# Kernel tuning notes

Hardware: AMD Instinct MI355X
Metric: run time of the kernel (lower is better)

## Reference

```python
import jax
import jax.numpy as jnp
from jax import lax
import numpy as np

B, T, IN, H, K = 8, 4096, 512, 512, 2


def setup_inputs() -> dict:
    key = jax.random.key(0)
    k = jax.random.split(key, 5)
    scale_w0 = 1.0 / np.sqrt(IN * K)
    scale_w1 = 1.0 / np.sqrt(H * K)
    return {
        "x": jax.random.normal(k[0], (B, T, IN), jnp.float32),
        "w0": jax.random.normal(k[1], (3 * H, IN, K), jnp.float32) * scale_w0,
        "b0": jax.random.normal(k[2], (3 * H,), jnp.float32) * scale_w0,
        "w1": jax.random.normal(k[3], (3 * H, H, K), jnp.float32) * scale_w1,
        "b1": jax.random.normal(k[4], (3 * H,), jnp.float32) * scale_w1,
    }


def _qrnn_layer(x, w, b):
    # x: [B, T, C]; w: [3H, C, K]; causal conv (left pad K-1), matching
    # torch padding=K-1 then slicing off the last K-1 timesteps.
    xc = jnp.transpose(x, (0, 2, 1))  # [B, C, T]
    conv = lax.conv_general_dilated(
        xc, w, window_strides=(1,), padding=[(K - 1, 0)],
        dimension_numbers=("NCH", "OIH", "NCH"))
    conv = conv + b[None, :, None]
    conv = jnp.transpose(conv, (0, 2, 1))  # [B, T, 3H]
    z, f, o = jnp.split(conv, 3, axis=-1)
    z = jnp.tanh(z)
    f = jax.nn.sigmoid(f)
    o = jax.nn.sigmoid(o)

    def step(h, zfo):
        zt, ft, ot = zfo
        h = ft * h + (1.0 - ft) * zt  # fo-pool recurrence
        return h, ot * h

    h0 = jnp.zeros((x.shape[0], z.shape[-1]), x.dtype)
    hT, outs = lax.scan(
        step, h0,
        (jnp.swapaxes(z, 0, 1), jnp.swapaxes(f, 0, 1), jnp.swapaxes(o, 0, 1)))
    return jnp.swapaxes(outs, 0, 1), hT  # [B, T, H], [B, H]


def reference(x, w0, b0, w1, b1):
    out, h0 = _qrnn_layer(x, w0, b0)
    out, h1 = _qrnn_layer(out, w1, b1)
    return out, h0, h1
```

## Files before the change

### kernel.cpp

```cpp
#include <hip/hip_runtime.h>
#include <cstdint>

#define B_ 8
#define T_ 4096
#define TP1 4097
#define IN_ 512
#define H_ 512
#define N3H 1536
#define KD 1024
#define CHUNKS 64
#define CLEN 64

typedef __attribute__((ext_vector_type(4))) float floatx4;
typedef __attribute__((ext_vector_type(4))) float f4;
typedef __attribute__((ext_vector_type(8))) short short8;
typedef __attribute__((ext_vector_type(4))) unsigned short us4;
typedef __attribute__((ext_vector_type(4))) _Float16 h4;

__device__ __forceinline__ unsigned short f2bf(float v){
  unsigned int u = __float_as_uint(v);
  unsigned int r = (u + 0x7fffu + ((u >> 16) & 1u)) >> 16;
  return (unsigned short)r;
}
__device__ __forceinline__ float sigm(float x){ return 1.f/(1.f + __expf(-x)); }
__device__ __forceinline__ float tanhf_(float x){ return 2.f*sigm(2.f*x) - 1.f; }

__global__ void cast_pad_kernel(const float* __restrict__ x, unsigned short* __restrict__ xpad){
  int64_t i = (int64_t)blockIdx.x*256 + threadIdx.x;
  const int64_t total = (int64_t)B_*TP1*(IN_/4);
  if (i >= total) return;
  int cg = (int)(i & 127);
  int64_t r = i >> 7;
  int t = (int)(r % TP1);
  int b = (int)(r / TP1);
  us4 o;
  if (t == 0){ o = (us4){0,0,0,0}; }
  else {
    f4 v = *(const f4*)(x + ((int64_t)b*T_ + (t-1))*IN_ + cg*4);
    #pragma unroll
    for (int u=0;u<4;++u) o[u] = f2bf(v[u]);
  }
  *(us4*)(xpad + r*IN_ + cg*4) = o;
}

__global__ void wt_kernel(const float* __restrict__ w, unsigned short* __restrict__ wt){
  int i = blockIdx.x*256 + threadIdx.x;
  if (i >= N3H*512) return;
  int ci = i & 511;
  int o = i >> 9;
  const float* wp = w + (int64_t)o*KD + ci*2;
  wt[(int64_t)o*KD + ci]       = f2bf(wp[0]);
  wt[(int64_t)o*KD + 512 + ci] = f2bf(wp[1]);
}

__global__ __launch_bounds__(256) void gemm_kernel(
    const unsigned short* __restrict__ A, const unsigned short* __restrict__ W,
    const float* __restrict__ bias, _Float16* __restrict__ C){
  __shared__ unsigned short As[128*32];
  __shared__ unsigned short Bs[128*32];
  const int tid = threadIdx.x;
  const int lane = tid & 63;
  const int wave = tid >> 6;
  const int bid = blockIdx.x;
  const int xcd = bid & 7;
  const int kb  = bid >> 3;
  const int colt = kb % 12;
  const int rowt = (kb / 12) * 8 + xcd;
  const int m0 = rowt * 128;
  const int n0 = colt * 128;
  const int bb = m0 / T_;
  const int act = n0 >> 9;
  const unsigned short* aSrc = A + (int64_t)(m0 + bb + (tid>>2))*IN_ + (tid&3)*8;
  const unsigned short* bSrc = W + (int64_t)(n0 + (tid>>2))*KD + (tid&3)*8;
  unsigned short* aDst = As + tid*8;
  unsigned short* bDst = Bs + tid*8;
  const int wm = wave & 1;
  const int wn = wave >> 1;
  const int l16 = lane & 15;
  const int quad = lane >> 4;
  floatx4 acc[4][4];
  #pragma unroll
  for (int i=0;i<4;i++)
    #pragma unroll
    for (int j=0;j<4;j++) acc[i][j] = (floatx4){0.f,0.f,0.f,0.f};
  const unsigned short* aLds = As + (wm*64 + l16)*32 + quad*8;
  const unsigned short* bLds = Bs + (wn*64 + l16)*32 + quad*8;

  for (int kk = 0; kk < KD; kk += 32){
    __syncthreads();
    __builtin_amdgcn_global_load_lds((const __attribute__((address_space(1))) void*)(aSrc + kk),
                                     (__attribute__((address_space(3))) void*)(aDst), 16, 0, 0);
    __builtin_amdgcn_global_load_lds((const __attribute__((address_space(1))) void*)(aSrc + 64*IN_ + kk),
                                     (__attribute__((address_space(3))) void*)(aDst + 2048), 16, 0, 0);
    __builtin_amdgcn_global_load_lds((const __attribute__((address_space(1))) void*)(bSrc + kk),
                                     (__attribute__((address_space(3))) void*)(bDst), 16, 0, 0);
    __builtin_amdgcn_global_load_lds((const __attribute__((address_space(1))) void*)(bSrc + 64*KD + kk),
                                     (__attribute__((address_space(3))) void*)(bDst + 2048), 16, 0, 0);
    __syncthreads();
    short8 af[4], bfr[4];
    #pragma unroll
    for (int i=0;i<4;i++) af[i] = *(const short8*)(aLds + i*16*32);
    #pragma unroll
    for (int j=0;j<4;j++) bfr[j] = *(const short8*)(bLds + j*16*32);
    #pragma unroll
    for (int i=0;i<4;i++)
      #pragma unroll
      for (int j=0;j<4;j++)
        acc[i][j] = __builtin_amdgcn_mfma_f32_16x16x32_bf16(af[i], bfr[j], acc[i][j], 0, 0, 0);
  }
  float bv[4];
  #pragma unroll
  for (int j=0;j<4;j++) bv[j] = bias[n0 + wn*64 + j*16 + l16];
  #pragma unroll
  for (int i=0;i<4;i++){
    int row = m0 + wm*64 + i*16 + quad*4;
    #pragma unroll
    for (int j=0;j<4;j++){
      int col = n0 + wn*64 + j*16 + l16;
      _Float16* cp = C + (int64_t)row*N3H + col;
      #pragma unroll
      for (int r=0;r<4;r++){
        float v = acc[i][j][r] + bv[j];
        v = (act == 0) ? tanhf_(v) : sigm(v);
        cp[(int64_t)r*N3H] = (_Float16)v;
      }
    }
  }
}

__global__ void scan_phase1(const _Float16* __restrict__ conv,
                            float* __restrict__ carA, float* __restrict__ carB){
  int q = blockIdx.x*256 + threadIdx.x;
  int chg = q & 127;
  int bq = (q >> 7) & 7;
  int c  = q >> 10;
  int ch = chg*4;
  f4 Aa = {1.f,1.f,1.f,1.f}, Bb = {0.f,0.f,0.f,0.f};
  const _Float16* p = conv + ((int64_t)bq*T_ + c*CLEN)*N3H + ch;
  for (int s=0;s<CLEN;++s){
    h4 zh = *(const h4*)p;
    h4 fh = *(const h4*)(p+512);
    #pragma unroll
    for (int u=0;u<4;++u){
      float fv = (float)fh[u];
      float zv = (float)zh[u];
      Aa[u] *= fv;
      Bb[u] = fv*Bb[u] + (1.f-fv)*zv;
    }
    p += N3H;
  }
  *(f4*)(carA + (int64_t)q*4) = Aa;
  *(f4*)(carB + (int64_t)q*4) = Bb;
}

__global__ void scan_phase2(const float* __restrict__ carA, const float* __restrict__ carB,
                            float* __restrict__ hstart, float* __restrict__ hT){
  int q = blockIdx.x*256 + threadIdx.x;
  f4 h = {0.f,0.f,0.f,0.f};
  for (int c=0;c<CHUNKS;++c){
    int64_t idx = (int64_t)c*4096 + q*4;
    *(f4*)(hstart + idx) = h;
    f4 a = *(const f4*)(carA + idx);
    f4 b = *(const f4*)(carB + idx);
    #pragma unroll
    for (int u=0;u<4;++u) h[u] = a[u]*h[u] + b[u];
  }
  *(f4*)(hT + (int64_t)q*4) = h;
}

template<int LAYER>
__global__ void scan_phase3(const _Float16* __restrict__ conv,
                            const float* __restrict__ hstart, unsigned short* __restrict__ xpad,
                            float* __restrict__ outf){
  int q = blockIdx.x*256 + threadIdx.x;
  int chg = q & 127;
  int bq = (q >> 7) & 7;
  int c  = q >> 10;
  int ch = chg*4;
  f4 h = *(const f4*)(hstart + (int64_t)q*4);
  const _Float16* p = conv + ((int64_t)bq*T_ + c*CLEN)*N3H + ch;
  int t = c*CLEN;
  for (int s=0;s<CLEN;++s){
    h4 zh = *(const h4*)p;
    h4 fh = *(const h4*)(p+512);
    h4 oh = *(const h4*)(p+1024);
    if (LAYER == 0){
      us4 ov4;
      #pragma unroll
      for (int u=0;u<4;++u){
        float fv = (float)fh[u];
        h[u] = fv*h[u] + (1.f-fv)*(float)zh[u];
        ov4[u] = f2bf((float)oh[u]*h[u]);
      }
      *(us4*)(xpad + ((int64_t)bq*TP1 + t + 1)*IN_ + ch) = ov4;
    } else {
      f4 of4;
      #pragma unroll
      for (int u=0;u<4;++u){
        float fv = (float)fh[u];
        h[u] = fv*h[u] + (1.f-fv)*(float)zh[u];
        of4[u] = (float)oh[u]*h[u];
      }
      *(f4*)(outf + ((int64_t)bq*T_ + t)*H_ + ch) = of4;
    }
    ++t; p += N3H;
  }
}

extern "C" void kernel_launch(void* const* d_in, const int* in_sizes, int n_in,
                              void* d_out, int out_size, void* d_ws, size_t ws_size,
                              hipStream_t stream){
  const float* x  = (const float*)d_in[0];
  const float* w0 = (const float*)d_in[1];
  const float* b0 = (const float*)d_in[2];
  const float* w1 = (const float*)d_in[3];
  const float* b1 = (const float*)d_in[4];
  float* out = (float*)d_out;

  char* ws = (char*)d_ws;
  size_t off = 0;
  auto alloc = [&](size_t bytes)->char*{
    char* p = ws + off; off = (off + bytes + 255) & ~(size_t)255; return p; };
  unsigned short* xpad = (unsigned short*)alloc((size_t)B_*TP1*IN_*2);
  unsigned short* Wt0  = (unsigned short*)alloc((size_t)N3H*KD*2);
  unsigned short* Wt1  = (unsigned short*)alloc((size_t)N3H*KD*2);
  _Float16* conv = (_Float16*)alloc((size_t)B_*T_*N3H*2);
  float* carA = (float*)alloc((size_t)CHUNKS*4096*4);
  float* carB = (float*)alloc((size_t)CHUNKS*4096*4);
  float* hst  = (float*)alloc((size_t)CHUNKS*4096*4);
  if (off > ws_size) return;

  float* out_main = out;
  float* h0 = out + (int64_t)B_*T_*H_;
  float* h1 = h0 + B_*H_;

  const int64_t padN = (int64_t)B_*TP1*(IN_/4);
  cast_pad_kernel<<<(int)((padN + 255)/256), 256, 0, stream>>>(x, xpad);
  wt_kernel<<<(N3H*512 + 255)/256, 256, 0, stream>>>(w0, Wt0);
  wt_kernel<<<(N3H*512 + 255)/256, 256, 0, stream>>>(w1, Wt1);

  const int ggrid = (N3H/128) * ((B_*T_)/128);
  gemm_kernel<<<ggrid, 256, 0, stream>>>(xpad, Wt0, b0, conv);
  scan_phase1<<<256, 256, 0, stream>>>(conv, carA, carB);
  scan_phase2<<<4, 256, 0, stream>>>(carA, carB, hst, h0);
  scan_phase3<0><<<256, 256, 0, stream>>>(conv, hst, xpad, nullptr);

  gemm_kernel<<<ggrid, 256, 0, stream>>>(xpad, Wt1, b1, conv);
  scan_phase1<<<256, 256, 0, stream>>>(conv, carA, carB);
  scan_phase2<<<4, 256, 0, stream>>>(carA, carB, hst, h1);
  scan_phase3<1><<<256, 256, 0, stream>>>(conv, hst, nullptr, out_main);
}
```

Measured before the change: 491.2 us.

## Double scan chunks, batch scan loads, widen GEMM K-step, merge weight casts

Splits the time scan into 128 chunks of 32 steps so the scan kernels launch twice as many blocks. The scan loops now issue 8 timesteps of loads before computing, to expose memory-level parallelism. The GEMM stages 64 K-elements per barrier pair using two LDS buffers, halving synchronisation count. The two weight-cast launches are fused into one via a 2D grid. Phase2 does twice as many serial steps and LDS use doubles.

Measured after the change: 499.3 us. No clear change (+1.6%).

```diff
diff --git a/kernel.cpp b/kernel.cpp
--- a/kernel.cpp
+++ b/kernel.cpp
@@ -8,8 +8,8 @@
 #define H_ 512
 #define N3H 1536
 #define KD 1024
-#define CHUNKS 64
-#define CLEN 64
+#define CHUNKS 128
+#define CLEN 32
 
 typedef __attribute__((ext_vector_type(4))) float floatx4;
 typedef __attribute__((ext_vector_type(4))) float f4;
@@ -24,6 +24,10 @@
 }
 __device__ __forceinline__ float sigm(float x){ return 1.f/(1.f + __expf(-x)); }
 __device__ __forceinline__ float tanhf_(float x){ return 2.f*sigm(2.f*x) - 1.f; }
+
+#define GLLS(src, dst) __builtin_amdgcn_global_load_lds( \
+    (const __attribute__((address_space(1))) void*)(src), \
+    (__attribute__((address_space(3))) void*)(dst), 16, 0, 0)
 
 __global__ void cast_pad_kernel(const float* __restrict__ x, unsigned short* __restrict__ xpad){
   int64_t i = (int64_t)blockIdx.x*256 + threadIdx.x;
@@ -43,9 +47,12 @@
   *(us4*)(xpad + r*IN_ + cg*4) = o;
 }
 
-__global__ void wt_kernel(const float* __restrict__ w, unsigned short* __restrict__ wt){
+__global__ void wt_kernel(const float* __restrict__ wA, unsigned short* __restrict__ wtA,
+                          const float* __restrict__ wB, unsigned short* __restrict__ wtB){
   int i = blockIdx.x*256 + threadIdx.x;
   if (i >= N3H*512) return;
+  const float* w = blockIdx.y ? wB : wA;
+  unsigned short* wt = blockIdx.y ? wtB : wtA;
   int ci = i & 511;
   int o = i >> 9;
   const float* wp = w + (int64_t)o*KD + ci*2;
@@ -56,8 +63,8 @@
 __global__ __launch_bounds__(256) void gemm_kernel(
     const unsigned short* __restrict__ A, const unsigned short* __restrict__ W,
     const float* __restrict__ bias, _Float16* __restrict__ C){
-  __shared__ unsigned short As[128*32];
-  __shared__ unsigned short Bs[128*32];
+  __shared__ unsigned short As[2][128*32];
+  __shared__ unsigned short Bs[2][128*32];
   const int tid = threadIdx.x;
   const int lane = tid & 63;
   const int wave = tid >> 6;
@@ -72,8 +79,10 @@
   const int act = n0 >> 9;
   const unsigned short* aSrc = A + (int64_t)(m0 + bb + (tid>>2))*IN_ + (tid&3)*8;
   const unsigned short* bSrc = W + (int64_t)(n0 + (tid>>2))*KD + (tid&3)*8;
-  unsigned short* aDst = As + tid*8;
-  unsigned short* bDst = Bs + tid*8;
+  unsigned short* aDst0 = As[0] + tid*8;
+  unsigned short* aDst1 = As[1] + tid*8;
+  unsigned short* bDst0 = Bs[0] + tid*8;
+  unsigned short* bDst1 = Bs[1] + tid*8;
   const int wm = wave & 1;
   const int wn = wave >> 1;
   const int l16 = lane & 15;
@@ -83,30 +92,35 @@
   for (int i=0;i<4;i++)
     #pragma unroll
     for (int j=0;j<4;j++) acc[i][j] = (floatx4){0.f,0.f,0.f,0.f};
-  const unsigned short* aLds = As + (wm*64 + l16)*32 + quad*8;
-  const unsigned short* bLds = Bs + (wn*64 + l16)*32 + quad*8;
-
-  for (int kk = 0; kk < KD; kk += 32){
+  const int fragOff = (wm*64 + l16)*32 + quad*8;
+  const int fragOffB = (wn*64 + l16)*32 + quad*8;
+
+  for (int kk = 0; kk < KD; kk += 64){
     __syncthreads();
-    __builtin_amdgcn_global_load_lds((const __attribute__((address_space(1))) void*)(aSrc + kk),
-                                     (__attribute__((address_space(3))) void*)(aDst), 16, 0, 0);
-    __builtin_amdgcn_global_load_lds((const __attribute__((address_space(1))) void*)(aSrc + 64*IN_ + kk),
-                                     (__attribute__((address_space(3))) void*)(aDst + 2048), 16, 0, 0);
-    __builtin_amdgcn_global_load_lds((const __attribute__((address_space(1))) void*)(bSrc + kk),
-                                     (__attribute__((address_space(3))) void*)(bDst), 16, 0, 0);
-    __builtin_amdgcn_global_load_lds((const __attribute__((address_space(1))) void*)(bSrc + 64*KD + kk),
-                                     (__attribute__((address_space(3))) void*)(bDst + 2048), 16, 0, 0);
+    GLLS(aSrc + kk,             aDst0);
+    GLLS(aSrc + 64*IN_ + kk,    aDst0 + 2048);
+    GLLS(aSrc + kk + 32,        aDst1);
+    GLLS(aSrc + 64*IN_ + kk+32, aDst1 + 2048);
+    GLLS(bSrc + kk,             bDst0);
+    GLLS(bSrc + 64*KD + kk,     bDst0 + 2048);
+    GLLS(bSrc + kk + 32,        bDst1);
+    GLLS(bSrc + 64*KD + kk+32,  bDst1 + 2048);
     __syncthreads();
-    short8 af[4], bfr[4];
-    #pragma unroll
-    for (int i=0;i<4;i++) af[i] = *(const short8*)(aLds + i*16*32);
-    #pragma unroll
-    for (int j=0;j<4;j++) bfr[j] = *(const short8*)(bLds + j*16*32);
-    #pragma unroll
-    for (int i=0;i<4;i++)
-      #pragma unroll
-      for (int j=0;j<4;j++)
-        acc[i][j] = __builtin_amdgcn_mfma_f32_16x16x32_bf16(af[i], bfr[j], acc[i][j], 0, 0, 0);
+    #pragma unroll
+    for (int s=0;s<2;++s){
+      const unsigned short* aLds = As[s] + fragOff;
+      const unsigned short* bLds = Bs[s] + fragOffB;
+      short8 af[4], bfr[4];
+      #pragma unroll
+      for (int i=0;i<4;i++) af[i] = *(const short8*)(aLds + i*16*32);
+      #pragma unroll
+      for (int j=0;j<4;j++) bfr[j] = *(const short8*)(bLds + j*16*32);
+      #pragma unroll
+      for (int i=0;i<4;i++)
+        #pragma unroll
+        for (int j=0;j<4;j++)
+          acc[i][j] = __builtin_amdgcn_mfma_f32_16x16x32_bf16(af[i], bfr[j], acc[i][j], 0, 0, 0);
+    }
   }
   float bv[4];
   #pragma unroll
@@ -137,17 +151,24 @@
   int ch = chg*4;
   f4 Aa = {1.f,1.f,1.f,1.f}, Bb = {0.f,0.f,0.f,0.f};
   const _Float16* p = conv + ((int64_t)bq*T_ + c*CLEN)*N3H + ch;
-  for (int s=0;s<CLEN;++s){
-    h4 zh = *(const h4*)p;
-    h4 fh = *(const h4*)(p+512);
-    #pragma unroll
-    for (int u=0;u<4;++u){
-      float fv = (float)fh[u];
-      float zv = (float)zh[u];
-      Aa[u] *= fv;
-      Bb[u] = fv*Bb[u] + (1.f-fv)*zv;
-    }
-    p += N3H;
+  for (int g=0; g<CLEN/8; ++g){
+    h4 zb[8], fb[8];
+    #pragma unroll
+    for (int u=0;u<8;++u){
+      zb[u] = *(const h4*)(p + (int64_t)u*N3H);
+      fb[u] = *(const h4*)(p + (int64_t)u*N3H + 512);
+    }
+    #pragma unroll
+    for (int u=0;u<8;++u){
+      #pragma unroll
+      for (int v=0;v<4;++v){
+        float fv = (float)fb[u][v];
+        float zv = (float)zb[u][v];
+        Aa[v] *= fv;
+        Bb[v] = fv*Bb[v] + (1.f-fv)*zv;
+      }
+    }
+    p += (int64_t)8*N3H;
   }
   *(f4*)(carA + (int64_t)q*4) = Aa;
   *(f4*)(carB + (int64_t)q*4) = Bb;
@@ -157,13 +178,21 @@
                             float* __restrict__ hstart, float* __restrict__ hT){
   int q = blockIdx.x*256 + threadIdx.x;
   f4 h = {0.f,0.f,0.f,0.f};
-  for (int c=0;c<CHUNKS;++c){
-    int64_t idx = (int64_t)c*4096 + q*4;
-    *(f4*)(hstart + idx) = h;
-    f4 a = *(const f4*)(carA + idx);
-    f4 b = *(const f4*)(carB + idx);
-    #pragma unroll
-    for (int u=0;u<4;++u) h[u] = a[u]*h[u] + b[u];
+  for (int g=0; g<CHUNKS/8; ++g){
+    f4 av[8], bv[8];
+    #pragma unroll
+    for (int u=0;u<8;++u){
+      int64_t idx = (int64_t)(g*8+u)*4096 + q*4;
+      av[u] = *(const f4*)(carA + idx);
+      bv[u] = *(const f4*)(carB + idx);
+    }
+    #pragma unroll
+    for (int u=0;u<8;++u){
+      int64_t idx = (int64_t)(g*8+u)*4096 + q*4;
+      *(f4*)(hstart + idx) = h;
+      #pragma unroll
+      for (int v=0;v<4;++v) h[v] = av[u][v]*h[v] + bv[u][v];
+    }
   }
   *(f4*)(hT + (int64_t)q*4) = h;
 }
@@ -180,30 +209,37 @@
   f4 h = *(const f4*)(hstart + (int64_t)q*4);
   const _Float16* p = conv + ((int64_t)bq*T_ + c*CLEN)*N3H + ch;
   int t = c*CLEN;
-  for (int s=0;s<CLEN;++s){
-    h4 zh = *(const h4*)p;
-    h4 fh = *(const h4*)(p+512);
-    h4 oh = *(const h4*)(p+1024);
-    if (LAYER == 0){
-      us4 ov4;
-      #pragma unroll
-      for (int u=0;u<4;++u){
-        float fv = (float)fh[u];
-        h[u] = fv*h[u] + (1.f-fv)*(float)zh[u];
-        ov4[u] = f2bf((float)oh[u]*h[u]);
+  for (int g=0; g<CLEN/8; ++g){
+    h4 zb[8], fb[8], ob[8];
+    #pragma unroll
+    for (int u=0;u<8;++u){
+      zb[u] = *(const h4*)(p + (int64_t)u*N3H);
+      fb[u] = *(const h4*)(p + (int64_t)u*N3H + 512);
+      ob[u] = *(const h4*)(p + (int64_t)u*N3H + 1024);
+    }
+    #pragma unroll
+    for (int u=0;u<8;++u){
+      if (LAYER == 0){
+        us4 ov4;
+        #pragma unroll
+        for (int v=0;v<4;++v){
+          float fv = (float)fb[u][v];
+          h[v] = fv*h[v] + (1.f-fv)*(float)zb[u][v];
+          ov4[v] = f2bf((float)ob[u][v]*h[v]);
+        }
+        *(us4*)(xpad + ((int64_t)bq*TP1 + t+u + 1)*IN_ + ch) = ov4;
+      } else {
+        f4 of4;
+        #pragma unroll
+        for (int v=0;v<4;++v){
+          float fv = (float)fb[u][v];
+          h[v] = fv*h[v] + (1.f-fv)*(float)zb[u][v];
+          of4[v] = (float)ob[u][v]*h[v];
+        }
+        *(f4*)(outf + ((int64_t)bq*T_ + t+u)*H_ + ch) = of4;
       }
-      *(us4*)(xpad + ((int64_t)bq*TP1 + t + 1)*IN_ + ch) = ov4;
-    } else {
-      f4 of4;
-      #pragma unroll
-      for (int u=0;u<4;++u){
-        float fv = (float)fh[u];
-        h[u] = fv*h[u] + (1.f-fv)*(float)zh[u];
-        of4[u] = (float)oh[u]*h[u];
-      }
-      *(f4*)(outf + ((int64_t)bq*T_ + t)*H_ + ch) = of4;
-    }
-    ++t; p += N3H;
+    }
+    t += 8; p += (int64_t)8*N3H;
   }
 }
 
@@ -236,17 +272,18 @@
 
   const int64_t padN = (int64_t)B_*TP1*(IN_/4);
   cast_pad_kernel<<<(int)((padN + 255)/256), 256, 0, stream>>>(x, xpad);
-  wt_kernel<<<(N3H*512 + 255)/256, 256, 0, stream>>>(w0, Wt0);
-  wt_kernel<<<(N3H*512 + 255)/256, 256, 0, stream>>>(w1, Wt1);
+  dim3 wgrid((N3H*512 + 255)/256, 2);
+  wt_kernel<<<wgrid, 256, 0, stream>>>(w0, Wt0, w1, Wt1);
 
   const int ggrid = (N3H/128) * ((B_*T_)/128);
+  const int sgrid = (CHUNKS*8*128) / 256;
   gemm_kernel<<<ggrid, 256, 0, stream>>>(xpad, Wt0, b0, conv);
-  scan_phase1<<<256, 256, 0, stream>>>(conv, carA, carB);
+  scan_phase1<<<sgrid, 256, 0, stream>>>(conv, carA, carB);
   scan_phase2<<<4, 256, 0, stream>>>(carA, carB, hst, h0);
-  scan_phase3<0><<<256, 256, 0, stream>>>(conv, hst, xpad, nullptr);
+  scan_phase3<0><<<sgrid, 256, 0, stream>>>(conv, hst, xpad, nullptr);
 
   gemm_kernel<<<ggrid, 256, 0, stream>>>(xpad, Wt1, b1, conv);
-  scan_phase1<<<256, 256, 0, stream>>>(conv, carA, carB);
+  scan_phase1<<<sgrid, 256, 0, stream>>>(conv, carA, carB);
   scan_phase2<<<4, 256, 0, stream>>>(carA, carB, hst, h1);
-  scan_phase3<1><<<256, 256, 0, stream>>>(conv, hst, nullptr, out_main);
-}
+  scan_phase3<1><<<sgrid, 256, 0, stream>>>(conv, hst, nullptr, out_main);
+}
```
